# Optimization experiments

Hardware: AMD Instinct MI355X
Metric: run time of the kernel (lower is better)

Reference implementation:

```python
import jax, jax.numpy as jnp
import numpy as np

B, L, D, V = 4, 512, 1024, 32000

def setup_inputs() -> dict:
    key = jax.random.key(0)
    k1, k2, k3 = jax.random.split(key, 3)
    cell = jax.random.normal(k1, (B, L, D), dtype=jnp.float32)
    cls_w = jax.random.normal(k2, (V, D), dtype=jnp.float32)
    labels = jax.random.randint(k3, (B, L), 0, V, dtype=jnp.int64)
    return {"cell": cell, "cls_w": cls_w, "labels": labels}

def reference(cell, cls_w, labels):
    # score: [B, L, V] = cell @ cls_w^T
    logits = jnp.einsum('bld,vd->blv', cell, cls_w)
    logits = logits.reshape(-1, logits.shape[-1])          # [B*L, V]
    tgt = labels.reshape(-1)                               # [B*L]
    logp = jax.nn.log_softmax(logits, axis=-1)             # stable log-softmax
    nll = -jnp.take_along_axis(logp, tgt[:, None], axis=-1)[:, 0]
    loss = jnp.mean(nll)                                   # CrossEntropyLoss default: mean
    return loss
```

## Files before the change

### kernel.cpp

```cpp
#include <hip/hip_runtime.h>

#define NROWS 2048
#define DIM   1024
#define VOCAB 32000
#define BM 256
#define BN 256
#define BK 64
#define NRB (NROWS / BM)
#define NVB (VOCAB / BN)
#define NCB (VOCAB / 64)
#define KSTEPS (DIM / BK)

typedef __attribute__((ext_vector_type(4))) float f32x4;
typedef __attribute__((ext_vector_type(8))) short bf16x8;
typedef unsigned int u32;

static __device__ inline unsigned short f2bf(float x) {
  union { float f; unsigned u; } c; c.f = x;
  unsigned r = c.u + 0x7fffu + ((c.u >> 16) & 1u);
  return (unsigned short)(r >> 16);
}

__global__ __launch_bounds__(256) void cvt_kernel(const float* __restrict__ in,
                                                  unsigned short* __restrict__ out) {
  int base = blockIdx.x * 512 + threadIdx.x;
  const float4* p = (const float4*)in;
  ushort4* o = (ushort4*)out;
  float4 v0 = p[base];
  float4 v1 = p[base + 256];
  ushort4 h0 = {f2bf(v0.x), f2bf(v0.y), f2bf(v0.z), f2bf(v0.w)};
  ushort4 h1 = {f2bf(v1.x), f2bf(v1.y), f2bf(v1.z), f2bf(v1.w)};
  o[base] = h0;
  o[base + 256] = h1;
}

__global__ __launch_bounds__(256) void tgt_kernel(
    const float* __restrict__ cell, const float* __restrict__ clsw,
    const int* __restrict__ labels, float* __restrict__ tlog) {
  int wv = threadIdx.x >> 6, lane = threadIdx.x & 63;
  int row = blockIdx.x * 4 + wv;
  int lbl = labels[row];
  const float4* a = (const float4*)(cell + (size_t)row * DIM);
  const float4* b = (const float4*)(clsw + (size_t)lbl * DIM);
  float acc = 0.f;
#pragma unroll
  for (int q = 0; q < 4; ++q) {
    float4 av = a[q * 64 + lane];
    float4 bv = b[q * 64 + lane];
    acc += av.x * bv.x + av.y * bv.y + av.z * bv.z + av.w * bv.w;
  }
#pragma unroll
  for (int off = 32; off >= 1; off >>= 1) acc += __shfl_xor(acc, off);
  if (lane == 0) tlog[row] = acc;
}

__global__ __launch_bounds__(512) void gemm_lse_kernel(
    const unsigned short* __restrict__ Ab, const unsigned short* __restrict__ Bb,
    float* __restrict__ partials) {
  __shared__ unsigned short smem[65536];

  const int h = blockIdx.x;
  const int g = (h & 7) * (NRB * NVB / 8) + (h >> 3);
  const int rb = g & (NRB - 1);
  const int vb = g >> 3;
  const int tid = threadIdx.x;
  const int wv = tid >> 6, lane = tid & 63;
  const int wr = wv >> 2, wc = wv & 3;
  const int lrow = lane & 15;
  const int lk = (lane >> 4) * 8;

  const size_t Abase = (size_t)rb * BM * DIM;
  const size_t Bbase = (size_t)vb * BN * DIM;

  f32x4 acc[8][4];
#pragma unroll
  for (int m = 0; m < 8; ++m)
#pragma unroll
    for (int n = 0; n < 4; ++n) acc[m][n] = (f32x4){0.f, 0.f, 0.f, 0.f};

  auto STAGE = [&](int kt, int buf) {
    unsigned short* As_ = smem + buf * 32768;
    unsigned short* Bs_ = As_ + 16384;
    const int kb = kt * BK;
#pragma unroll
    for (int q = 0; q < 4; ++q) {
      const int t = wv * 4 + q;
      const int rt = t >> 1, ks = t & 1;
      const size_t off = (size_t)(rt * 16 + lrow) * DIM + kb + ks * 32 + lk;
      __builtin_amdgcn_global_load_lds(
          (const __attribute__((address_space(1))) u32*)(Ab + Abase + off),
          (__attribute__((address_space(3))) u32*)(As_ + t * 512), 16, 0, 0);
      __builtin_amdgcn_global_load_lds(
          (const __attribute__((address_space(1))) u32*)(Bb + Bbase + off),
          (__attribute__((address_space(3))) u32*)(Bs_ + t * 512), 16, 0, 0);
    }
  };

  auto COMPUTE = [&](int buf) {
    const unsigned short* As_ = smem + buf * 32768;
    const unsigned short* Bs_ = As_ + 16384;
    __builtin_amdgcn_s_setprio(1);
#pragma unroll
    for (int ks = 0; ks < 2; ++ks) {
      bf16x8 b[4];
#pragma unroll
      for (int n = 0; n < 4; ++n)
        b[n] = *(const bf16x8*)(Bs_ + ((wc * 4 + n) * 2 + ks) * 512 + lane * 8);
#pragma unroll
      for (int m = 0; m < 8; ++m) {
        bf16x8 a = *(const bf16x8*)(As_ + ((wr * 8 + m) * 2 + ks) * 512 + lane * 8);
#pragma unroll
        for (int n = 0; n < 4; ++n)
          acc[m][n] = __builtin_amdgcn_mfma_f32_16x16x32_bf16(a, b[n], acc[m][n], 0, 0, 0);
      }
    }
    __builtin_amdgcn_s_setprio(0);
  };

  STAGE(0, 0);
  for (int kt = 0; kt < KSTEPS - 1; ++kt) {
    const int cur = kt & 1;
    STAGE(kt + 1, cur ^ 1);
    asm volatile("s_waitcnt vmcnt(8)" ::: "memory");
    __builtin_amdgcn_sched_barrier(0);
    __builtin_amdgcn_s_barrier();
    __builtin_amdgcn_sched_barrier(0);
    COMPUTE(cur);
    asm volatile("s_waitcnt lgkmcnt(0)" ::: "memory");
    __builtin_amdgcn_sched_barrier(0);
    __builtin_amdgcn_s_barrier();
    __builtin_amdgcn_sched_barrier(0);
  }
  asm volatile("s_waitcnt vmcnt(0)" ::: "memory");
  __builtin_amdgcn_sched_barrier(0);
  __builtin_amdgcn_s_barrier();
  __builtin_amdgcn_sched_barrier(0);
  COMPUTE((KSTEPS - 1) & 1);

#pragma unroll
  for (int m = 0; m < 8; ++m) {
#pragma unroll
    for (int i = 0; i < 4; ++i) {
      float mx = acc[m][0][i];
#pragma unroll
      for (int n = 1; n < 4; ++n) mx = fmaxf(mx, acc[m][n][i]);
      float s = 0.f;
#pragma unroll
      for (int n = 0; n < 4; ++n) s += __expf(acc[m][n][i] - mx);
#pragma unroll
      for (int off = 1; off <= 8; off <<= 1) {
        float om = __shfl_xor(mx, off);
        float os = __shfl_xor(s, off);
        float nm = fmaxf(mx, om);
        s = s * __expf(mx - nm) + os * __expf(om - nm);
        mx = nm;
      }
      if ((lane & 15) == 0) {
        int grow = rb * BM + wr * 128 + m * 16 + (lane >> 4) * 4 + i;
        int cb = vb * 4 + wc;
        *(float2*)(partials + ((size_t)grow * NCB + cb) * 2) = make_float2(mx, s);
      }
    }
  }
}

__global__ __launch_bounds__(256) void reduce_kernel(
    const float* __restrict__ partials, const float* __restrict__ tlog,
    float* __restrict__ out) {
  int wv = threadIdx.x >> 6, lane = threadIdx.x & 63;
  int row = blockIdx.x * 4 + wv;
  const float2* p = (const float2*)(partials + (size_t)row * NCB * 2);
  float m = -1e30f, s = 0.f;
  for (int i = lane; i < NCB; i += 64) {
    float2 v = p[i];
    float nm = fmaxf(m, v.x);
    s = s * __expf(m - nm) + v.y * __expf(v.x - nm);
    m = nm;
  }
#pragma unroll
  for (int off = 1; off <= 32; off <<= 1) {
    float om = __shfl_xor(m, off);
    float os = __shfl_xor(s, off);
    float nm = fmaxf(m, om);
    s = s * __expf(m - nm) + os * __expf(om - nm);
    m = nm;
  }
  float loss = m + __logf(s) - tlog[row];
  __shared__ float red[4];
  if (lane == 0) red[wv] = loss;
  __syncthreads();
  if (threadIdx.x == 0)
    atomicAdd(out, (red[0] + red[1] + red[2] + red[3]) * (1.0f / NROWS));
}

extern "C" void kernel_launch(void* const* d_in, const int* in_sizes, int n_in,
                              void* d_out, int out_size, void* d_ws, size_t ws_size,
                              hipStream_t stream) {
  const float* cell = (const float*)d_in[0];
  const float* clsw = (const float*)d_in[1];
  const int* labels = (const int*)d_in[2];
  float* out = (float*)d_out;

  unsigned short* cellb = (unsigned short*)d_ws;
  unsigned short* clswb = (unsigned short*)((char*)d_ws + 4194304);
  float* tlog = (float*)((char*)d_ws + 69730304);
  float* partials = (float*)((char*)d_ws + 69738496);

  hipMemsetAsync(out, 0, sizeof(float), stream);
  cvt_kernel<<<(NROWS * DIM / 4) / 512, 256, 0, stream>>>(cell, cellb);
  cvt_kernel<<<(VOCAB * DIM / 4) / 512, 256, 0, stream>>>(clsw, clswb);
  tgt_kernel<<<NROWS / 4, 256, 0, stream>>>(cell, clsw, labels, tlog);
  gemm_lse_kernel<<<NRB * NVB, 512, 0, stream>>>(cellb, clswb, partials);
  reduce_kernel<<<NROWS / 4, 256, 0, stream>>>(partials, tlog, out);
}
```

Before: 404.1 us.

## Fuse convert, target-logit, GEMM-LSE and reduce into one cooperative persistent kernel

Replaces five launches and a memset with a single cooperative kernel of 256 blocks. Grid syncs separate three phases: the bf16 conversion plus target-logit dot products, a persistent loop over the GEMM+LSE tiles, and the final reduction. The K-loop is also reworked to stage half-tiles per ks step and to load LDS fragments before issuing the next prefetch. This is meant to remove launch gaps and improve load/MFMA overlap. The risks are grid-sync overhead, losing the swizzled tile order, and register pressure from the (512, 2) launch bound forcing a large accumulator array into a smaller register budget.

```diff
diff --git a/kernel.cpp b/kernel.cpp
--- a/kernel.cpp
+++ b/kernel.cpp
@@ -1,4 +1,7 @@
 #include <hip/hip_runtime.h>
+#include <hip/hip_cooperative_groups.h>
+
+namespace cg = cooperative_groups;
 
 #define NROWS 2048
 #define DIM   1024
@@ -8,8 +11,11 @@
 #define BK 64
 #define NRB (NROWS / BM)
 #define NVB (VOCAB / BN)
+#define NJOBS (NRB * NVB)
 #define NCB (VOCAB / 64)
 #define KSTEPS (DIM / BK)
+#define NBLK 256
+#define NTHR 512
 
 typedef __attribute__((ext_vector_type(4))) float f32x4;
 typedef __attribute__((ext_vector_type(8))) short bf16x8;
@@ -21,176 +27,172 @@
   return (unsigned short)(r >> 16);
 }
 
-__global__ __launch_bounds__(256) void cvt_kernel(const float* __restrict__ in,
-                                                  unsigned short* __restrict__ out) {
-  int base = blockIdx.x * 512 + threadIdx.x;
-  const float4* p = (const float4*)in;
-  ushort4* o = (ushort4*)out;
-  float4 v0 = p[base];
-  float4 v1 = p[base + 256];
-  ushort4 h0 = {f2bf(v0.x), f2bf(v0.y), f2bf(v0.z), f2bf(v0.w)};
-  ushort4 h1 = {f2bf(v1.x), f2bf(v1.y), f2bf(v1.z), f2bf(v1.w)};
-  o[base] = h0;
-  o[base + 256] = h1;
-}
-
-__global__ __launch_bounds__(256) void tgt_kernel(
+__global__ __launch_bounds__(NTHR, 2) void fused_kernel(
     const float* __restrict__ cell, const float* __restrict__ clsw,
-    const int* __restrict__ labels, float* __restrict__ tlog) {
-  int wv = threadIdx.x >> 6, lane = threadIdx.x & 63;
-  int row = blockIdx.x * 4 + wv;
-  int lbl = labels[row];
-  const float4* a = (const float4*)(cell + (size_t)row * DIM);
-  const float4* b = (const float4*)(clsw + (size_t)lbl * DIM);
-  float acc = 0.f;
-#pragma unroll
-  for (int q = 0; q < 4; ++q) {
-    float4 av = a[q * 64 + lane];
-    float4 bv = b[q * 64 + lane];
-    acc += av.x * bv.x + av.y * bv.y + av.z * bv.z + av.w * bv.w;
-  }
-#pragma unroll
-  for (int off = 32; off >= 1; off >>= 1) acc += __shfl_xor(acc, off);
-  if (lane == 0) tlog[row] = acc;
-}
-
-__global__ __launch_bounds__(512) void gemm_lse_kernel(
-    const unsigned short* __restrict__ Ab, const unsigned short* __restrict__ Bb,
-    float* __restrict__ partials) {
+    const int* __restrict__ labels, float* __restrict__ out,
+    unsigned short* __restrict__ cellb, unsigned short* __restrict__ clswb,
+    float* __restrict__ tlog, float* __restrict__ partials) {
   __shared__ unsigned short smem[65536];
-
-  const int h = blockIdx.x;
-  const int g = (h & 7) * (NRB * NVB / 8) + (h >> 3);
-  const int rb = g & (NRB - 1);
-  const int vb = g >> 3;
   const int tid = threadIdx.x;
   const int wv = tid >> 6, lane = tid & 63;
-  const int wr = wv >> 2, wc = wv & 3;
-  const int lrow = lane & 15;
-  const int lk = (lane >> 4) * 8;
-
-  const size_t Abase = (size_t)rb * BM * DIM;
-  const size_t Bbase = (size_t)vb * BN * DIM;
-
-  f32x4 acc[8][4];
-#pragma unroll
-  for (int m = 0; m < 8; ++m)
-#pragma unroll
-    for (int n = 0; n < 4; ++n) acc[m][n] = (f32x4){0.f, 0.f, 0.f, 0.f};
-
-  auto STAGE = [&](int kt, int buf) {
-    unsigned short* As_ = smem + buf * 32768;
-    unsigned short* Bs_ = As_ + 16384;
-    const int kb = kt * BK;
+  const int gtid = blockIdx.x * NTHR + tid;
+
+  if (gtid == 0) out[0] = 0.f;
+  {
+    const float4* src = (const float4*)cell;
+    ushort4* dst = (ushort4*)cellb;
+    for (int i = gtid; i < NROWS * DIM / 4; i += NBLK * NTHR) {
+      float4 v = src[i];
+      ushort4 h = {f2bf(v.x), f2bf(v.y), f2bf(v.z), f2bf(v.w)};
+      dst[i] = h;
+    }
+    src = (const float4*)clsw;
+    dst = (ushort4*)clswb;
+    for (int i = gtid; i < VOCAB * DIM / 4; i += NBLK * NTHR) {
+      float4 v = src[i];
+      ushort4 h = {f2bf(v.x), f2bf(v.y), f2bf(v.z), f2bf(v.w)};
+      dst[i] = h;
+    }
+  }
+  {
+    int row = blockIdx.x * 8 + wv;
+    int lbl = labels[row];
+    const float4* a = (const float4*)(cell + (size_t)row * DIM);
+    const float4* b = (const float4*)(clsw + (size_t)lbl * DIM);
+    float acc = 0.f;
 #pragma unroll
     for (int q = 0; q < 4; ++q) {
-      const int t = wv * 4 + q;
-      const int rt = t >> 1, ks = t & 1;
-      const size_t off = (size_t)(rt * 16 + lrow) * DIM + kb + ks * 32 + lk;
-      __builtin_amdgcn_global_load_lds(
-          (const __attribute__((address_space(1))) u32*)(Ab + Abase + off),
-          (__attribute__((address_space(3))) u32*)(As_ + t * 512), 16, 0, 0);
-      __builtin_amdgcn_global_load_lds(
-          (const __attribute__((address_space(1))) u32*)(Bb + Bbase + off),
-          (__attribute__((address_space(3))) u32*)(Bs_ + t * 512), 16, 0, 0);
-    }
-  };
-
-  auto COMPUTE = [&](int buf) {
-    const unsigned short* As_ = smem + buf * 32768;
-    const unsigned short* Bs_ = As_ + 16384;
-    __builtin_amdgcn_s_setprio(1);
-#pragma unroll
-    for (int ks = 0; ks < 2; ++ks) {
-      bf16x8 b[4];
-#pragma unroll
-      for (int n = 0; n < 4; ++n)
-        b[n] = *(const bf16x8*)(Bs_ + ((wc * 4 + n) * 2 + ks) * 512 + lane * 8);
+      float4 av = a[q * 64 + lane];
+      float4 bv = b[q * 64 + lane];
+      acc += av.x * bv.x + av.y * bv.y + av.z * bv.z + av.w * bv.w;
+    }
+#pragma unroll
+    for (int off = 32; off >= 1; off >>= 1) acc += __shfl_xor(acc, off);
+    if (lane == 0) tlog[row] = acc;
+  }
+  __threadfence();
+  cg::this_grid().sync();
+
+  {
+    const int wr = wv >> 2, wc = wv & 3;
+    const int lrow = lane & 15, lk = (lane >> 4) * 8;
+
+    for (int g = blockIdx.x; g < NJOBS; g += NBLK) {
+      const int rb = g & (NRB - 1);
+      const int vb = g >> 3;
+      const size_t Abase = (size_t)rb * BM * DIM;
+      const size_t Bbase = (size_t)vb * BN * DIM;
+
+      f32x4 acc[8][4];
+#pragma unroll
+      for (int m = 0; m < 8; ++m)
+#pragma unroll
+        for (int n = 0; n < 4; ++n) acc[m][n] = (f32x4){0.f, 0.f, 0.f, 0.f};
+
+      auto STAGE_CHUNK = [&](int kt, int buf, int ks) {
+        unsigned short* As_ = smem + buf * 32768;
+        unsigned short* Bs_ = As_ + 16384;
+        const int kb = kt * BK + ks * 32 + lk;
+#pragma unroll
+        for (int q = 0; q < 2; ++q) {
+          const int rt = wv * 2 + q;
+          const int t = rt * 2 + ks;
+          const size_t off = (size_t)(rt * 16 + lrow) * DIM + kb;
+          __builtin_amdgcn_global_load_lds(
+              (const __attribute__((address_space(1))) u32*)(cellb + Abase + off),
+              (__attribute__((address_space(3))) u32*)(As_ + t * 512), 16, 0, 0);
+          __builtin_amdgcn_global_load_lds(
+              (const __attribute__((address_space(1))) u32*)(clswb + Bbase + off),
+              (__attribute__((address_space(3))) u32*)(Bs_ + t * 512), 16, 0, 0);
+        }
+      };
+
+      STAGE_CHUNK(0, 0, 0);
+      STAGE_CHUNK(0, 0, 1);
+
+      for (int kt = 0; kt < KSTEPS; ++kt) {
+        const int cur = kt & 1;
+#pragma unroll
+        for (int ks = 0; ks < 2; ++ks) {
+          if (kt == KSTEPS - 1 && ks == 1)
+            asm volatile("s_waitcnt vmcnt(0)" ::: "memory");
+          else
+            asm volatile("s_waitcnt vmcnt(4)" ::: "memory");
+          __builtin_amdgcn_sched_barrier(0);
+          __builtin_amdgcn_s_barrier();
+          __builtin_amdgcn_sched_barrier(0);
+
+          const unsigned short* As_ = smem + cur * 32768;
+          const unsigned short* Bs_ = As_ + 16384;
+          bf16x8 b[4], a[8];
+#pragma unroll
+          for (int n = 0; n < 4; ++n)
+            b[n] = *(const bf16x8*)(Bs_ + ((wc * 4 + n) * 2 + ks) * 512 + lane * 8);
+#pragma unroll
+          for (int m = 0; m < 8; ++m)
+            a[m] = *(const bf16x8*)(As_ + ((wr * 8 + m) * 2 + ks) * 512 + lane * 8);
+          if (kt < KSTEPS - 1) STAGE_CHUNK(kt + 1, cur ^ 1, ks);
+          __builtin_amdgcn_s_setprio(1);
+#pragma unroll
+          for (int m = 0; m < 8; ++m)
+#pragma unroll
+            for (int n = 0; n < 4; ++n)
+              acc[m][n] = __builtin_amdgcn_mfma_f32_16x16x32_bf16(a[m], b[n], acc[m][n], 0, 0, 0);
+          __builtin_amdgcn_s_setprio(0);
+        }
+      }
+
 #pragma unroll
       for (int m = 0; m < 8; ++m) {
-        bf16x8 a = *(const bf16x8*)(As_ + ((wr * 8 + m) * 2 + ks) * 512 + lane * 8);
-#pragma unroll
-        for (int n = 0; n < 4; ++n)
-          acc[m][n] = __builtin_amdgcn_mfma_f32_16x16x32_bf16(a, b[n], acc[m][n], 0, 0, 0);
+#pragma unroll
+        for (int i = 0; i < 4; ++i) {
+          float mx = acc[m][0][i];
+#pragma unroll
+          for (int n = 1; n < 4; ++n) mx = fmaxf(mx, acc[m][n][i]);
+          float s = 0.f;
+#pragma unroll
+          for (int n = 0; n < 4; ++n) s += __expf(acc[m][n][i] - mx);
+#pragma unroll
+          for (int off = 1; off <= 8; off <<= 1) {
+            float om = __shfl_xor(mx, off);
+            float os = __shfl_xor(s, off);
+            float nm = fmaxf(mx, om);
+            s = s * __expf(mx - nm) + os * __expf(om - nm);
+            mx = nm;
+          }
+          if ((lane & 15) == 0) {
+            int grow = rb * BM + wr * 128 + m * 16 + (lane >> 4) * 4 + i;
+            int cb = vb * 4 + wc;
+            *(float2*)(partials + ((size_t)grow * NCB + cb) * 2) = make_float2(mx, s);
+          }
+        }
       }
     }
-    __builtin_amdgcn_s_setprio(0);
-  };
-
-  STAGE(0, 0);
-  for (int kt = 0; kt < KSTEPS - 1; ++kt) {
-    const int cur = kt & 1;
-    STAGE(kt + 1, cur ^ 1);
-    asm volatile("s_waitcnt vmcnt(8)" ::: "memory");
-    __builtin_amdgcn_sched_barrier(0);
-    __builtin_amdgcn_s_barrier();
-    __builtin_amdgcn_sched_barrier(0);
-    COMPUTE(cur);
-    asm volatile("s_waitcnt lgkmcnt(0)" ::: "memory");
-    __builtin_amdgcn_sched_barrier(0);
-    __builtin_amdgcn_s_barrier();
-    __builtin_amdgcn_sched_barrier(0);
-  }
-  asm volatile("s_waitcnt vmcnt(0)" ::: "memory");
-  __builtin_amdgcn_sched_barrier(0);
-  __builtin_amdgcn_s_barrier();
-  __builtin_amdgcn_sched_barrier(0);
-  COMPUTE((KSTEPS - 1) & 1);
-
-#pragma unroll
-  for (int m = 0; m < 8; ++m) {
-#pragma unroll
-    for (int i = 0; i < 4; ++i) {
-      float mx = acc[m][0][i];
-#pragma unroll
-      for (int n = 1; n < 4; ++n) mx = fmaxf(mx, acc[m][n][i]);
-      float s = 0.f;
-#pragma unroll
-      for (int n = 0; n < 4; ++n) s += __expf(acc[m][n][i] - mx);
-#pragma unroll
-      for (int off = 1; off <= 8; off <<= 1) {
-        float om = __shfl_xor(mx, off);
-        float os = __shfl_xor(s, off);
-        float nm = fmaxf(mx, om);
-        s = s * __expf(mx - nm) + os * __expf(om - nm);
-        mx = nm;
-      }
-      if ((lane & 15) == 0) {
-        int grow = rb * BM + wr * 128 + m * 16 + (lane >> 4) * 4 + i;
-        int cb = vb * 4 + wc;
-        *(float2*)(partials + ((size_t)grow * NCB + cb) * 2) = make_float2(mx, s);
-      }
-    }
-  }
-}
-
-__global__ __launch_bounds__(256) void reduce_kernel(
-    const float* __restrict__ partials, const float* __restrict__ tlog,
-    float* __restrict__ out) {
-  int wv = threadIdx.x >> 6, lane = threadIdx.x & 63;
-  int row = blockIdx.x * 4 + wv;
-  const float2* p = (const float2*)(partials + (size_t)row * NCB * 2);
-  float m = -1e30f, s = 0.f;
-  for (int i = lane; i < NCB; i += 64) {
-    float2 v = p[i];
-    float nm = fmaxf(m, v.x);
-    s = s * __expf(m - nm) + v.y * __expf(v.x - nm);
-    m = nm;
-  }
-#pragma unroll
-  for (int off = 1; off <= 32; off <<= 1) {
-    float om = __shfl_xor(m, off);
-    float os = __shfl_xor(s, off);
-    float nm = fmaxf(m, om);
-    s = s * __expf(m - nm) + os * __expf(om - nm);
-    m = nm;
-  }
-  float loss = m + __logf(s) - tlog[row];
-  __shared__ float red[4];
-  if (lane == 0) red[wv] = loss;
-  __syncthreads();
-  if (threadIdx.x == 0)
-    atomicAdd(out, (red[0] + red[1] + red[2] + red[3]) * (1.0f / NROWS));
+  }
+  __threadfence();
+  cg::this_grid().sync();
+
+  {
+    int row = blockIdx.x * 8 + wv;
+    const float2* p = (const float2*)(partials + (size_t)row * NCB * 2);
+    float m = -1e30f, s = 0.f;
+    for (int i = lane; i < NCB; i += 64) {
+      float2 v = p[i];
+      float nm = fmaxf(m, v.x);
+      s = s * __expf(m - nm) + v.y * __expf(v.x - nm);
+      m = nm;
+    }
+#pragma unroll
+    for (int off = 1; off <= 32; off <<= 1) {
+      float om = __shfl_xor(m, off);
+      float os = __shfl_xor(s, off);
+      float nm = fmaxf(m, om);
+      s = s * __expf(m - nm) + os * __expf(om - nm);
+      m = nm;
+    }
+    if (lane == 0)
+      atomicAdd(out, (m + __logf(s) - tlog[row]) * (1.0f / NROWS));
+  }
 }
 
 extern "C" void kernel_launch(void* const* d_in, const int* in_sizes, int n_in,
@@ -206,10 +208,7 @@
   float* tlog = (float*)((char*)d_ws + 69730304);
   float* partials = (float*)((char*)d_ws + 69738496);
 
-  hipMemsetAsync(out, 0, sizeof(float), stream);
-  cvt_kernel<<<(NROWS * DIM / 4) / 512, 256, 0, stream>>>(cell, cellb);
-  cvt_kernel<<<(VOCAB * DIM / 4) / 512, 256, 0, stream>>>(clsw, clswb);
-  tgt_kernel<<<NROWS / 4, 256, 0, stream>>>(cell, clsw, labels, tlog);
-  gemm_lse_kernel<<<NRB * NVB, 512, 0, stream>>>(cellb, clswb, partials);
-  reduce_kernel<<<NROWS / 4, 256, 0, stream>>>(partials, tlog, out);
+  void* args[] = {&cell, &clsw, &labels, &out, &cellb, &clswb, &tlog, &partials};
+  hipLaunchCooperativeKernel((void*)fused_kernel, dim3(NBLK), dim3(NTHR),
+                             args, 0, stream);
 }
```

After: 604.3 us. 49.5% more time.
